# Performance work log

Measured on AMD Instinct MI355X. Metric: run time of the kernel, lower is better.

Reference implementation:

```python
import jax, jax.numpy as jnp
import numpy as np

NUM_REGIONS = 116
EPS = 1e-6
GAMMA = 1e-3


def setup_inputs() -> dict:
    key = jax.random.key(0)
    k1, k2, k3 = jax.random.split(key, 3)
    shape = (16, 3, 512, 512)
    real = jax.random.normal(k1, shape, dtype=jnp.float32)
    fake = jax.random.normal(k2, shape, dtype=jnp.float32)
    region_map = jax.random.randint(k3, shape, 0, NUM_REGIONS, dtype=jnp.int32)
    return {"real": real, "fake": fake, "region_map": region_map}


def reference(real, fake, region_map):
    # Elementwise L1 loss (reduction='none')
    whole_loss = jnp.abs(real - fake)

    flat_ids = region_map.reshape(-1)
    flat_loss = whole_loss.reshape(-1)

    # per-region sum of loss and per-region element count.
    sums = jax.ops.segment_sum(flat_loss, flat_ids, num_segments=NUM_REGIONS)
    counts = jax.ops.segment_sum(
        jnp.ones_like(flat_loss), flat_ids, num_segments=NUM_REGIONS
    )
    rloss_mean = sums / (counts + EPS)  # [116]

    # max_l1_loss buffer starts at 0 and takes running max of detached means;
    # after the first loop it equals max(0, max_r rloss_mean), with no grad.
    max_l1 = jnp.maximum(jnp.max(jax.lax.stop_gradient(rloss_mean)), 0.0)

    # Per-region weight (rloss_mean NOT detached here, so grads flow through it)
    w = 1.0 + GAMMA * (rloss_mean / (max_l1 + EPS))  # [116]

    # sum_r w_r * (whole_loss * mask_r) == whole_loss * w[region_map]
    weighted = whole_loss * w[region_map]
    return weighted.mean()
```

## Files before the change

kernel.cpp:

```cpp
#include <hip/hip_runtime.h>

#define NUM_REGIONS 116
#define EPS 1e-6f
#define GAMMA 1e-3f

#define SUM_SCALE 2048.0f
#define CNT32_SHIFT 21
#define SUM32_MASK ((1u << CNT32_SHIFT) - 1u)

#define FIX_INV   (1.0f / 2048.0f)
#define CNT_SHIFT 40
#define SUM_MASK  ((1ULL << CNT_SHIFT) - 1ULL)

typedef unsigned long long u64;
typedef unsigned int u32;

__global__ __launch_bounds__(256) void region_accum_kernel(
    const float* __restrict__ real,
    const float* __restrict__ fake,
    const int*   __restrict__ rmap,
    u64* __restrict__ g_acc,
    int n, int n4)
{
    __shared__ u32 s_acc[4][NUM_REGIONS];
    const int tid = threadIdx.x;
    u32* tbl = s_acc[tid >> 6];

    for (int i = tid; i < 4 * NUM_REGIONS; i += 256)
        (&s_acc[0][0])[i] = 0u;
    __syncthreads();

    const float4* real4 = (const float4*)real;
    const float4* fake4 = (const float4*)fake;
    const int4*   map4  = (const int4*)rmap;

    const int stride = gridDim.x * 256;
    for (int i = blockIdx.x * 256 + tid; i < n4; i += stride) {
        float4 a = real4[i];
        float4 b = fake4[i];
        int4   m = map4[i];
        u32 vx = (1u << CNT32_SHIFT) | (u32)(fabsf(a.x - b.x) * SUM_SCALE + 0.5f);
        u32 vy = (1u << CNT32_SHIFT) | (u32)(fabsf(a.y - b.y) * SUM_SCALE + 0.5f);
        u32 vz = (1u << CNT32_SHIFT) | (u32)(fabsf(a.z - b.z) * SUM_SCALE + 0.5f);
        u32 vw = (1u << CNT32_SHIFT) | (u32)(fabsf(a.w - b.w) * SUM_SCALE + 0.5f);
        atomicAdd(&tbl[m.x], vx);
        atomicAdd(&tbl[m.y], vy);
        atomicAdd(&tbl[m.z], vz);
        atomicAdd(&tbl[m.w], vw);
    }

    const int tail = n4 << 2;
    if (blockIdx.x == 0 && tid < (n - tail)) {
        int idx = tail + tid;
        u32 v = (1u << CNT32_SHIFT) |
                (u32)(fabsf(real[idx] - fake[idx]) * SUM_SCALE + 0.5f);
        atomicAdd(&tbl[rmap[idx]], v);
    }
    __syncthreads();

    for (int r = tid; r < NUM_REGIONS; r += 256) {
        u64 sum = 0, cnt = 0;
#pragma unroll
        for (int k = 0; k < 4; ++k) {
            u32 v = s_acc[k][r];
            sum += (u64)(v & SUM32_MASK);
            cnt += (u64)(v >> CNT32_SHIFT);
        }
        u64 packed = (cnt << CNT_SHIFT) | sum;
        if (packed) atomicAdd(&g_acc[r], packed);
    }
}

__global__ __launch_bounds__(64) void region_finalize_kernel(
    const u64* __restrict__ g_acc,
    float* __restrict__ out,
    float inv_n)
{
    const int lane = threadIdx.x;
    u64 tA = g_acc[lane];
    float sA = (float)(tA & SUM_MASK) * FIX_INV;
    float cA = (float)(tA >> CNT_SHIFT);
    float mA = sA / (cA + EPS);

    float sB = 0.0f, mB = 0.0f;
    if (lane + 64 < NUM_REGIONS) {
        u64 tB = g_acc[lane + 64];
        sB = (float)(tB & SUM_MASK) * FIX_INV;
        float cB = (float)(tB >> CNT_SHIFT);
        mB = sB / (cB + EPS);
    }

    float mx = fmaxf(mA, mB);
#pragma unroll
    for (int off = 32; off > 0; off >>= 1)
        mx = fmaxf(mx, __shfl_xor(mx, off));
    mx = fmaxf(mx, 0.0f);

    const float k = GAMMA / (mx + EPS);
    float part = sA * (1.0f + mA * k) + sB * (1.0f + mB * k);
#pragma unroll
    for (int off = 32; off > 0; off >>= 1)
        part += __shfl_xor(part, off);

    if (lane == 0)
        out[0] = part * inv_n;
}

extern "C" void kernel_launch(void* const* d_in, const int* in_sizes, int n_in,
                              void* d_out, int out_size, void* d_ws, size_t ws_size,
                              hipStream_t stream) {
    const float* real = (const float*)d_in[0];
    const float* fake = (const float*)d_in[1];
    const int*   rmap = (const int*)d_in[2];
    float* out = (float*)d_out;

    const int n  = in_sizes[0];
    const int n4 = n >> 2;

    u64* g_acc = (u64*)d_ws;
    hipMemsetAsync(d_ws, 0, NUM_REGIONS * sizeof(u64), stream);

    int blocks = (n4 + 255) / 256;
    if (blocks > 2048) blocks = 2048;
    if (blocks < 1) blocks = 1;

    region_accum_kernel<<<blocks, 256, 0, stream>>>(real, fake, rmap, g_acc, n, n4);
    region_finalize_kernel<<<1, 64, 0, stream>>>(g_acc, out, 1.0f / (float)n);
}
```

Before: 183.1 us.

## Replace shared-memory atomics with per-lane private LDS histograms and prefetching

The accumulation kernel drops shared-memory atomicAdd on four 116-entry tables. Each block is now a single 64-thread wave, and every lane owns its own column of a [116][64] LDS histogram, updated with plain read-modify-write that has no atomics and no bank conflicts. Each block handles a fixed 12 iterations and software-prefetches the next float4 group, and the packed fixed-point layout moves to a 4096 scale with a 24-bit sum field. The cost is about 30 KB of LDS per one-wave block, which limits waves per CU, plus a per-block 64-column reduction and many more blocks issuing global atomics.

```diff
diff --git a/kernel.cpp b/kernel.cpp
--- a/kernel.cpp
+++ b/kernel.cpp
@@ -4,70 +4,89 @@
 #define EPS 1e-6f
 #define GAMMA 1e-3f
 
-#define SUM_SCALE 2048.0f
-#define CNT32_SHIFT 21
+#define SUM_SCALE 4096.0f
+#define CNT32_SHIFT 24
 #define SUM32_MASK ((1u << CNT32_SHIFT) - 1u)
 
-#define FIX_INV   (1.0f / 2048.0f)
+#define FIX_INV   (1.0f / 4096.0f)
 #define CNT_SHIFT 40
 #define SUM_MASK  ((1ULL << CNT_SHIFT) - 1ULL)
+
+#define ITERS 12
+#define GROUPS_PER_BLOCK (64 * ITERS)
 
 typedef unsigned long long u64;
 typedef unsigned int u32;
 
-__global__ __launch_bounds__(256) void region_accum_kernel(
+__global__ __launch_bounds__(64) void region_accum_kernel(
     const float* __restrict__ real,
     const float* __restrict__ fake,
     const int*   __restrict__ rmap,
     u64* __restrict__ g_acc,
     int n, int n4)
 {
-    __shared__ u32 s_acc[4][NUM_REGIONS];
-    const int tid = threadIdx.x;
-    u32* tbl = s_acc[tid >> 6];
+    __shared__ u32 hist[NUM_REGIONS][64];
+    const int lane = threadIdx.x;
 
-    for (int i = tid; i < 4 * NUM_REGIONS; i += 256)
-        (&s_acc[0][0])[i] = 0u;
+    {
+        uint4 z = make_uint4(0, 0, 0, 0);
+        uint4* p = (uint4*)&hist[0][0];
+        for (int i = lane; i < (NUM_REGIONS * 64) / 4; i += 64)
+            p[i] = z;
+    }
     __syncthreads();
 
     const float4* real4 = (const float4*)real;
     const float4* fake4 = (const float4*)fake;
     const int4*   map4  = (const int4*)rmap;
 
-    const int stride = gridDim.x * 256;
-    for (int i = blockIdx.x * 256 + tid; i < n4; i += stride) {
-        float4 a = real4[i];
-        float4 b = fake4[i];
-        int4   m = map4[i];
-        u32 vx = (1u << CNT32_SHIFT) | (u32)(fabsf(a.x - b.x) * SUM_SCALE + 0.5f);
-        u32 vy = (1u << CNT32_SHIFT) | (u32)(fabsf(a.y - b.y) * SUM_SCALE + 0.5f);
-        u32 vz = (1u << CNT32_SHIFT) | (u32)(fabsf(a.z - b.z) * SUM_SCALE + 0.5f);
-        u32 vw = (1u << CNT32_SHIFT) | (u32)(fabsf(a.w - b.w) * SUM_SCALE + 0.5f);
-        atomicAdd(&tbl[m.x], vx);
-        atomicAdd(&tbl[m.y], vy);
-        atomicAdd(&tbl[m.z], vz);
-        atomicAdd(&tbl[m.w], vw);
+    const int base = blockIdx.x * GROUPS_PER_BLOCK + lane;
+
+#define RMW(av, bv, mv) { \
+        u32* p = &hist[0][0] + (u32)(mv) * 64u + (u32)lane; \
+        *p += (1u << CNT32_SHIFT) | (u32)(fabsf((av) - (bv)) * SUM_SCALE + 0.5f); }
+
+    int idx = base;
+    bool v0 = idx < n4;
+    float4 a, b; int4 m;
+    if (v0) { a = real4[idx]; b = fake4[idx]; m = map4[idx]; }
+
+    for (int j = 0; j < ITERS; ++j) {
+        int nidx = base + 64 * (j + 1);
+        bool vn = (j + 1 < ITERS) && (nidx < n4);
+        float4 an, bn; int4 mn;
+        if (vn) { an = real4[nidx]; bn = fake4[nidx]; mn = map4[nidx]; }
+
+        if (v0) {
+            RMW(a.x, b.x, m.x);
+            RMW(a.y, b.y, m.y);
+            RMW(a.z, b.z, m.z);
+            RMW(a.w, b.w, m.w);
+        }
+        a = an; b = bn; m = mn; v0 = vn;
     }
 
     const int tail = n4 << 2;
-    if (blockIdx.x == 0 && tid < (n - tail)) {
-        int idx = tail + tid;
-        u32 v = (1u << CNT32_SHIFT) |
-                (u32)(fabsf(real[idx] - fake[idx]) * SUM_SCALE + 0.5f);
-        atomicAdd(&tbl[rmap[idx]], v);
+    if (blockIdx.x == 0 && lane < (n - tail)) {
+        int i2 = tail + lane;
+        RMW(real[i2], fake[i2], rmap[i2]);
     }
+#undef RMW
     __syncthreads();
 
-    for (int r = tid; r < NUM_REGIONS; r += 256) {
-        u64 sum = 0, cnt = 0;
+    for (int pass = 0; pass < 2; ++pass) {
+        int r = lane + pass * 64;
+        if (r < NUM_REGIONS) {
+            u32 cnt = 0, sum = 0;
 #pragma unroll
-        for (int k = 0; k < 4; ++k) {
-            u32 v = s_acc[k][r];
-            sum += (u64)(v & SUM32_MASK);
-            cnt += (u64)(v >> CNT32_SHIFT);
+            for (int j = 0; j < 64; ++j) {
+                u32 v = hist[r][(lane + j) & 63];
+                cnt += v >> CNT32_SHIFT;
+                sum += v & SUM32_MASK;
+            }
+            u64 packed = ((u64)cnt << CNT_SHIFT) | (u64)sum;
+            if (packed) atomicAdd(&g_acc[r], packed);
         }
-        u64 packed = (cnt << CNT_SHIFT) | sum;
-        if (packed) atomicAdd(&g_acc[r], packed);
     }
 }
 
@@ -120,10 +139,9 @@
     u64* g_acc = (u64*)d_ws;
     hipMemsetAsync(d_ws, 0, NUM_REGIONS * sizeof(u64), stream);
 
-    int blocks = (n4 + 255) / 256;
-    if (blocks > 2048) blocks = 2048;
+    int blocks = (n4 + GROUPS_PER_BLOCK - 1) / GROUPS_PER_BLOCK;
     if (blocks < 1) blocks = 1;
 
-    region_accum_kernel<<<blocks, 256, 0, stream>>>(real, fake, rmap, g_acc, n, n4);
+    region_accum_kernel<<<blocks, 64, 0, stream>>>(real, fake, rmap, g_acc, n, n4);
     region_finalize_kernel<<<1, 64, 0, stream>>>(g_acc, out, 1.0f / (float)n);
 }
```

Measured after the change: 225.6 us. 1.23x slower.
